# Kernel optimization log

Measured on AMD Instinct MI355X. Metric: run time of the kernel, lower is better.

## Reference

```python
import jax, jax.numpy as jnp
import numpy as np

N = 20000
M = 32          # max_neighbors
IN_DIM = 256
OUT_DIM = 256
H = 4           # num_heads
D = OUT_DIM // H  # head_dim = 64
LN_EPS = 1e-5
NEG_INF = -1.0e9


def setup_inputs() -> dict:
    key = jax.random.key(0)
    ks = jax.random.split(key, 6)
    h = jax.random.normal(ks[0], (N, IN_DIM), dtype=jnp.float32)
    neighbor_idx = jax.random.randint(ks[1], (N, M), 0, N, dtype=jnp.int32)
    neighbor_mask = jax.random.randint(ks[2], (N, M), 0, 2, dtype=jnp.int32)
    # parameters (xavier-ish scaling)
    W = jax.random.normal(ks[3], (IN_DIM, OUT_DIM), dtype=jnp.float32) / np.sqrt(IN_DIM)
    a_l = jax.random.normal(ks[4], (H, D), dtype=jnp.float32) / np.sqrt(D)
    a_r = jax.random.normal(ks[5], (H, D), dtype=jnp.float32) / np.sqrt(D)
    ln_gamma = jnp.ones((OUT_DIM,), dtype=jnp.float32)
    ln_beta = jnp.zeros((OUT_DIM,), dtype=jnp.float32)
    return {"h": h, "neighbor_idx": neighbor_idx, "neighbor_mask": neighbor_mask,
            "W": W, "a_l": a_l, "a_r": a_r, "ln_gamma": ln_gamma, "ln_beta": ln_beta}


def reference(h, neighbor_idx, neighbor_mask, W, a_l, a_r, ln_gamma, ln_beta):
    h_proj = h @ W                                   # [N, OUT_DIM]
    h_heads = h_proj.reshape(N, H, D)                # [N, H, D]
    # per-node score halves; gathering scalars instead of full features for er
    el = jnp.einsum('nhd,hd->nh', h_heads, a_l)      # [N, H]
    er_node = jnp.einsum('nhd,hd->nh', h_heads, a_r) # [N, H]
    er = er_node[neighbor_idx]                       # [N, M, H]
    e = jax.nn.leaky_relu(el[:, None, :] + er, negative_slope=0.2)  # [N, M, H]
    e = jnp.where(neighbor_mask[:, :, None] == 0, NEG_INF, e)
    alpha = jax.nn.softmax(e, axis=1)                # softmax over neighbors
    neigh_h = h_heads[neighbor_idx]                  # [N, M, H, D]
    out_heads = jnp.einsum('nmh,nmhd->nhd', alpha, neigh_h)
    H_cat = out_heads.reshape(N, OUT_DIM)
    res = h_proj                                     # in_dim == out_dim -> res_proj is None
    out = jax.nn.gelu(H_cat + res, approximate=False)
    # LayerNorm over last dim
    mu = jnp.mean(out, axis=-1, keepdims=True)
    var = jnp.var(out, axis=-1, keepdims=True)
    out = (out - mu) * jax.lax.rsqrt(var + LN_EPS) * ln_gamma + ln_beta
    return out
```

## Files before the change

### kernel.cpp

```cpp
#include <hip/hip_runtime.h>
#include <math.h>

#define N_NODES 20000
#define M_NEI   32
#define DIM     256
#define H_HEADS 4
#define D_HEAD  64
#define LN_EPS  1e-5f
#define NEG_INF -1.0e9f
#define APAD    264
#define NB      8

using short8  = __attribute__((ext_vector_type(8))) short;
using short4v = __attribute__((ext_vector_type(4))) short;
using floatx4 = __attribute__((ext_vector_type(4))) float;
using floatx2 = __attribute__((ext_vector_type(2))) float;
using uintx4  = __attribute__((ext_vector_type(4))) unsigned int;

__device__ __forceinline__ float bf2f(unsigned short u) {
    union { unsigned int i; float f; } c; c.i = ((unsigned int)u) << 16; return c.f;
}
__device__ __forceinline__ float u2f(unsigned int i) {
    union { unsigned int i; float f; } c; c.i = i; return c.f;
}
__device__ __forceinline__ unsigned short f2bf(float f) {
    union { float f; unsigned int i; } c; c.f = f;
    unsigned int x = c.i;
    x += 0x7fffu + ((x >> 16) & 1u);
    return (unsigned short)(x >> 16);
}
__device__ __forceinline__ bool in_is_fp32(const void* gamma) {
    return *(const unsigned int*)gamma == 0x3F800000u;
}
__device__ __forceinline__ float fast_exp(float x) {
    return __builtin_amdgcn_exp2f(x * 1.44269504088896341f);
}

__global__ __launch_bounds__(256, 2) void k_gemm(const void* __restrict__ A,
                                                 const void* __restrict__ gamma,
                                                 const void* __restrict__ W,
                                                 const void* __restrict__ al,
                                                 const void* __restrict__ ar,
                                                 unsigned short* __restrict__ hp,
                                                 float* __restrict__ el_nh,
                                                 float* __restrict__ er_nh) {
    __shared__ unsigned short sA[32][APAD];
    const bool f32 = in_is_fp32(gamma);
    const int t    = threadIdx.x;
    const int m0   = blockIdx.x * 32;
    const int hd   = t >> 6;
    const int lane = t & 63;
    const int r    = lane & 15;
    const int quad = lane >> 4;
    const int n0   = hd * 64;

    short8 breg[4][8];
    if (f32) {
        #pragma unroll
        for (int c = 0; c < 4; ++c) {
            const float* wp = (const float*)W + (size_t)quad * 8 * DIM + n0 + c * 16 + r;
            #pragma unroll
            for (int kq = 0; kq < 8; ++kq) {
                #pragma unroll
                for (int j = 0; j < 8; ++j)
                    breg[c][kq][j] = (short)f2bf(wp[(size_t)(kq * 32 + j) * DIM]);
            }
        }
    } else {
        #pragma unroll
        for (int c = 0; c < 4; ++c) {
            const unsigned short* wp = (const unsigned short*)W + (size_t)quad * 8 * DIM + n0 + c * 16 + r;
            #pragma unroll
            for (int kq = 0; kq < 8; ++kq) {
                #pragma unroll
                for (int j = 0; j < 8; ++j)
                    breg[c][kq][j] = (short)wp[(size_t)(kq * 32 + j) * DIM];
            }
        }
    }

    #pragma unroll
    for (int it = 0; it < 4; ++it) {
        int chunk = it * 256 + t;
        int row   = chunk >> 5;
        int c16   = chunk & 31;
        short8 v;
        if (!f32) {
            v = *(const short8*)((const unsigned short*)A + (size_t)(m0 + row) * DIM + c16 * 8);
        } else {
            const float* ap = (const float*)A + (size_t)(m0 + row) * DIM + c16 * 8;
            floatx4 f0 = *(const floatx4*)ap;
            floatx4 f1 = *(const floatx4*)(ap + 4);
            #pragma unroll
            for (int j = 0; j < 4; ++j) {
                v[j]     = (short)f2bf(f0[j]);
                v[4 + j] = (short)f2bf(f1[j]);
            }
        }
        *(short8*)&sA[row][c16 * 8] = v;
    }
    __syncthreads();

    floatx4 acc[2][4];
    #pragma unroll
    for (int rf = 0; rf < 2; ++rf)
        #pragma unroll
        for (int c = 0; c < 4; ++c) acc[rf][c] = (floatx4){0.f, 0.f, 0.f, 0.f};

    #pragma unroll
    for (int kq = 0; kq < 8; ++kq) {
        short8 a0 = *(const short8*)&sA[r][kq * 32 + quad * 8];
        short8 a1 = *(const short8*)&sA[16 + r][kq * 32 + quad * 8];
        #pragma unroll
        for (int c = 0; c < 4; ++c) {
            acc[0][c] = __builtin_amdgcn_mfma_f32_16x16x32_bf16(a0, breg[c][kq], acc[0][c], 0, 0, 0);
            acc[1][c] = __builtin_amdgcn_mfma_f32_16x16x32_bf16(a1, breg[c][kq], acc[1][c], 0, 0, 0);
        }
    }

    float alv[4], arv[4];
    #pragma unroll
    for (int c = 0; c < 4; ++c) {
        int col = n0 + c * 16 + r;
        if (f32) { alv[c] = ((const float*)al)[col]; arv[c] = ((const float*)ar)[col]; }
        else     { alv[c] = bf2f(((const unsigned short*)al)[col]);
                   arv[c] = bf2f(((const unsigned short*)ar)[col]); }
    }

    #pragma unroll
    for (int rf = 0; rf < 2; ++rf) {
        #pragma unroll
        for (int rr = 0; rr < 4; ++rr) {
            const int row = m0 + rf * 16 + quad * 4 + rr;
            float sl = 0.f, sr = 0.f;
            #pragma unroll
            for (int c = 0; c < 4; ++c) {
                float v = acc[rf][c][rr];
                sl += v * alv[c];
                sr += v * arv[c];
                hp[(size_t)row * DIM + n0 + c * 16 + r] = f2bf(v);
            }
            #pragma unroll
            for (int off = 1; off < 16; off <<= 1) {
                sl += __shfl_xor(sl, off);
                sr += __shfl_xor(sr, off);
            }
            if (r == 0) {
                el_nh[(size_t)row * H_HEADS + hd] = sl;
                er_nh[(size_t)row * H_HEADS + hd] = sr;
            }
        }
    }
}

__global__ __launch_bounds__(256) void k_fuse(const int* __restrict__ nidx,
                                              const int* __restrict__ nmask,
                                              const unsigned short* __restrict__ hp,
                                              const float* __restrict__ el_nh,
                                              const float* __restrict__ er_nh,
                                              const void* __restrict__ gamma,
                                              const void* __restrict__ beta,
                                              void* __restrict__ out) {
    __shared__ int   s_off[NB][33];
    __shared__ float s_al[NB][33][4];
    __shared__ int   s_cnt[NB];

    const int t   = threadIdx.x;
    const int nb0 = blockIdx.x * NB;

    {
        int*     offp = &s_off[0][0];
        floatx4* alp  = (floatx4*)&s_al[0][0][0];
        if (t < NB * 33) {
            offp[t] = 0;
            alp[t]  = (floatx4){0.f, 0.f, 0.f, 0.f};
        }
        if (t < NB * 33 - 256) {
            offp[256 + t] = 0;
            alp[256 + t]  = (floatx4){0.f, 0.f, 0.f, 0.f};
        }
    }
    __syncthreads();

    {
        const int m   = t & 31;
        const int nl  = t >> 5;
        const int n   = nb0 + nl;
        const int idx = nidx[(size_t)n * M_NEI + m];
        const int msk = nmask[(size_t)n * M_NEI + m];
        floatx4 el4 = *(const floatx4*)(el_nh + (size_t)n * H_HEADS);
        floatx4 er4 = *(const floatx4*)(er_nh + (size_t)idx * H_HEADS);
        floatx4 e4, a4;
        #pragma unroll
        for (int hh = 0; hh < 4; ++hh) {
            float e = el4[hh] + er4[hh];
            e = (e > 0.f) ? e : 0.2f * e;
            e4[hh] = msk ? e : NEG_INF;
        }
        floatx4 mx = e4;
        #pragma unroll
        for (int off = 1; off < 32; off <<= 1)
            #pragma unroll
            for (int hh = 0; hh < 4; ++hh)
                mx[hh] = fmaxf(mx[hh], __shfl_xor(mx[hh], off, 32));
        #pragma unroll
        for (int hh = 0; hh < 4; ++hh) a4[hh] = fast_exp(e4[hh] - mx[hh]);
        floatx4 sm = a4;
        #pragma unroll
        for (int off = 1; off < 32; off <<= 1)
            #pragma unroll
            for (int hh = 0; hh < 4; ++hh)
                sm[hh] += __shfl_xor(sm[hh], off, 32);
        #pragma unroll
        for (int hh = 0; hh < 4; ++hh) a4[hh] *= __builtin_amdgcn_rcpf(sm[hh]);

        unsigned long long bal64 = __ballot(msk != 0);
        unsigned int bal = (t & 32) ? (unsigned int)(bal64 >> 32)
                                    : (unsigned int)bal64;
        int  cnt   = __popc(bal);
        bool valid = (msk != 0);
        if (cnt == 0) { valid = true; cnt = 32; bal = 0xffffffffu; }
        if (valid) {
            int pfx = __popc(bal & ((1u << m) - 1u));
            s_off[nl][pfx] = idx * (DIM * 2);
            *(floatx4*)&s_al[nl][pfx][0] = a4;
        }
        if (m == 0) s_cnt[nl] = cnt;
    }
    __syncthreads();

    const bool f32 = in_is_fp32(gamma);
    const int nl   = t >> 5;
    const int l32  = t & 31;
    const int hq   = l32 >> 3;
    const int n    = nb0 + nl;
    const int cnt  = s_cnt[nl];
    const char* tbl = (const char*)hp + (size_t)l32 * 16;

    float gv[8], bv[8];
    if (f32) {
        #pragma unroll
        for (int i = 0; i < 8; ++i) {
            gv[i] = ((const float*)gamma)[l32 * 8 + i];
            bv[i] = ((const float*)beta)[l32 * 8 + i];
        }
    } else {
        #pragma unroll
        for (int i = 0; i < 8; ++i) {
            gv[i] = bf2f(((const unsigned short*)gamma)[l32 * 8 + i]);
            bv[i] = bf2f(((const unsigned short*)beta)[l32 * 8 + i]);
        }
    }

    floatx2 acc[4];
    #pragma unroll
    for (int j = 0; j < 4; ++j) acc[j] = (floatx2){0.f, 0.f};

    for (int m = 0; m < cnt; m += 4) {
        #pragma unroll
        for (int k = 0; k < 4; ++k) {
            const int   off = s_off[nl][m + k];
            const float aa  = s_al[nl][m + k][hq];
            uintx4 u = *(const uintx4*)(tbl + off);
            #pragma unroll
            for (int j = 0; j < 4; ++j) {
                floatx2 f = { u2f(u[j] << 16), u2f(u[j] & 0xffff0000u) };
                acc[j] += (floatx2){aa, aa} * f;
            }
        }
    }

    {
        uintx4 u = *(const uintx4*)((const char*)hp + (size_t)n * (DIM * 2) + l32 * 16);
        #pragma unroll
        for (int j = 0; j < 4; ++j) {
            floatx2 f = { u2f(u[j] << 16), u2f(u[j] & 0xffff0000u) };
            acc[j] += f;
        }
    }

    float x[8], s1 = 0.f, s2 = 0.f;
    #pragma unroll
    for (int j = 0; j < 4; ++j) {
        #pragma unroll
        for (int e = 0; e < 2; ++e) {
            float xi = acc[j][e];
            xi = 0.5f * xi * (1.f + erff(xi * 0.70710678118654752f));
            x[2 * j + e] = xi;
            s1 += xi;
            s2 += xi * xi;
        }
    }
    #pragma unroll
    for (int off = 1; off < 32; off <<= 1) {
        s1 += __shfl_xor(s1, off, 32);
        s2 += __shfl_xor(s2, off, 32);
    }
    const float mu  = s1 * (1.f / 256.f);
    float var = s2 * (1.f / 256.f) - mu * mu;
    var = fmaxf(var, 0.f);
    const float inv = rsqrtf(var + LN_EPS);

    if (f32) {
        float* op = (float*)out + (size_t)n * DIM + l32 * 8;
        floatx4 o0, o1;
        #pragma unroll
        for (int i = 0; i < 4; ++i) {
            o0[i] = (x[i]     - mu) * inv * gv[i]     + bv[i];
            o1[i] = (x[4 + i] - mu) * inv * gv[4 + i] + bv[4 + i];
        }
        *(floatx4*)op       = o0;
        *(floatx4*)(op + 4) = o1;
    } else {
        short8 o;
        #pragma unroll
        for (int i = 0; i < 8; ++i)
            o[i] = (short)f2bf((x[i] - mu) * inv * gv[i] + bv[i]);
        *(short8*)((unsigned short*)out + (size_t)n * DIM + l32 * 8) = o;
    }
}

extern "C" void kernel_launch(void* const* d_in, const int* in_sizes, int n_in,
                              void* d_out, int out_size, void* d_ws, size_t ws_size,
                              hipStream_t stream) {
    const void* h     = d_in[0];
    const int*  nidx  = (const int*)d_in[1];
    const int*  nmask = (const int*)d_in[2];
    const void* W     = d_in[3];
    const void* al    = d_in[4];
    const void* ar    = d_in[5];
    const void* gamma = d_in[6];
    const void* beta  = d_in[7];

    unsigned short* hp    = (unsigned short*)d_ws;
    float* el_nh = (float*)((char*)d_ws + 10240000);
    float* er_nh = (float*)((char*)d_ws + 10560000);

    k_gemm<<<N_NODES / 32, 256, 0, stream>>>(h, gamma, W, al, ar, hp, el_nh, er_nh);
    k_fuse<<<N_NODES / NB, 256, 0, stream>>>(nidx, nmask, hp, el_nh, er_nh,
                                             gamma, beta, d_out);
}
```

Measured before the change: 127.7 us.

## Use one wavefront per node in aggregation and a fast erf approximation

The aggregation kernel now processes 4 nodes per block with a full 64-lane wavefront per node, each lane gathering 8 bytes (4 bf16) instead of 16 bytes across 32 lanes. This doubles thread-level parallelism per node for the gather and shortens per-thread work, at the cost of more blocks and a longer 64-lane reduction. It also replaces erff with an Abramowitz-Stegun polynomial plus exp2, which reduces transcendental cost but adds approximation error of about 1e-7 absolute.

```diff
diff --git a/kernel.cpp b/kernel.cpp
--- a/kernel.cpp
+++ b/kernel.cpp
@@ -9,13 +9,14 @@
 #define LN_EPS  1e-5f
 #define NEG_INF -1.0e9f
 #define APAD    264
-#define NB      8
+#define NB      4
 
 using short8  = __attribute__((ext_vector_type(8))) short;
 using short4v = __attribute__((ext_vector_type(4))) short;
 using floatx4 = __attribute__((ext_vector_type(4))) float;
 using floatx2 = __attribute__((ext_vector_type(2))) float;
 using uintx4  = __attribute__((ext_vector_type(4))) unsigned int;
+using uintx2  = __attribute__((ext_vector_type(2))) unsigned int;
 
 __device__ __forceinline__ float bf2f(unsigned short u) {
     union { unsigned int i; float f; } c; c.i = ((unsigned int)u) << 16; return c.f;
@@ -34,6 +35,18 @@
 }
 __device__ __forceinline__ float fast_exp(float x) {
     return __builtin_amdgcn_exp2f(x * 1.44269504088896341f);
+}
+__device__ __forceinline__ float erf_fast(float x) {
+    float ax = fabsf(x);
+    float t  = __builtin_amdgcn_rcpf(fmaf(0.3275911f, ax, 1.0f));
+    float p  = fmaf(1.061405429f, t, -1.453152027f);
+    p = fmaf(p, t, 1.421413741f);
+    p = fmaf(p, t, -0.284496736f);
+    p = fmaf(p, t, 0.254829592f);
+    p = p * t;
+    float e  = __builtin_amdgcn_exp2f(-ax * ax * 1.44269504088896341f);
+    float r  = fmaf(-p, e, 1.0f);
+    return copysignf(r, x);
 }
 
 __global__ __launch_bounds__(256, 2) void k_gemm(const void* __restrict__ A,
@@ -175,14 +188,10 @@
             offp[t] = 0;
             alp[t]  = (floatx4){0.f, 0.f, 0.f, 0.f};
         }
-        if (t < NB * 33 - 256) {
-            offp[256 + t] = 0;
-            alp[256 + t]  = (floatx4){0.f, 0.f, 0.f, 0.f};
-        }
     }
     __syncthreads();
 
-    {
+    if (t < NB * 32) {
         const int m   = t & 31;
         const int nl  = t >> 5;
         const int n   = nb0 + nl;
@@ -230,40 +239,40 @@
     __syncthreads();
 
     const bool f32 = in_is_fp32(gamma);
-    const int nl   = t >> 5;
-    const int l32  = t & 31;
-    const int hq   = l32 >> 3;
+    const int nl   = t >> 6;
+    const int lane = t & 63;
+    const int hq   = lane >> 4;
     const int n    = nb0 + nl;
     const int cnt  = s_cnt[nl];
-    const char* tbl = (const char*)hp + (size_t)l32 * 16;
-
-    float gv[8], bv[8];
+    const char* tbl = (const char*)hp + (size_t)lane * 8;
+
+    float gv[4], bv[4];
     if (f32) {
         #pragma unroll
-        for (int i = 0; i < 8; ++i) {
-            gv[i] = ((const float*)gamma)[l32 * 8 + i];
-            bv[i] = ((const float*)beta)[l32 * 8 + i];
+        for (int i = 0; i < 4; ++i) {
+            gv[i] = ((const float*)gamma)[lane * 4 + i];
+            bv[i] = ((const float*)beta)[lane * 4 + i];
         }
     } else {
         #pragma unroll
-        for (int i = 0; i < 8; ++i) {
-            gv[i] = bf2f(((const unsigned short*)gamma)[l32 * 8 + i]);
-            bv[i] = bf2f(((const unsigned short*)beta)[l32 * 8 + i]);
-        }
-    }
-
-    floatx2 acc[4];
-    #pragma unroll
-    for (int j = 0; j < 4; ++j) acc[j] = (floatx2){0.f, 0.f};
+        for (int i = 0; i < 4; ++i) {
+            gv[i] = bf2f(((const unsigned short*)gamma)[lane * 4 + i]);
+            bv[i] = bf2f(((const unsigned short*)beta)[lane * 4 + i]);
+        }
+    }
+
+    floatx2 acc[2];
+    acc[0] = (floatx2){0.f, 0.f};
+    acc[1] = (floatx2){0.f, 0.f};
 
     for (int m = 0; m < cnt; m += 4) {
         #pragma unroll
         for (int k = 0; k < 4; ++k) {
             const int   off = s_off[nl][m + k];
             const float aa  = s_al[nl][m + k][hq];
-            uintx4 u = *(const uintx4*)(tbl + off);
-            #pragma unroll
-            for (int j = 0; j < 4; ++j) {
+            uintx2 u = *(const uintx2*)(tbl + off);
+            #pragma unroll
+            for (int j = 0; j < 2; ++j) {
                 floatx2 f = { u2f(u[j] << 16), u2f(u[j] & 0xffff0000u) };
                 acc[j] += (floatx2){aa, aa} * f;
             }
@@ -271,30 +280,30 @@
     }
 
     {
-        uintx4 u = *(const uintx4*)((const char*)hp + (size_t)n * (DIM * 2) + l32 * 16);
-        #pragma unroll
-        for (int j = 0; j < 4; ++j) {
+        uintx2 u = *(const uintx2*)((const char*)hp + (size_t)n * (DIM * 2) + lane * 8);
+        #pragma unroll
+        for (int j = 0; j < 2; ++j) {
             floatx2 f = { u2f(u[j] << 16), u2f(u[j] & 0xffff0000u) };
             acc[j] += f;
         }
     }
 
-    float x[8], s1 = 0.f, s2 = 0.f;
-    #pragma unroll
-    for (int j = 0; j < 4; ++j) {
+    float x[4], s1 = 0.f, s2 = 0.f;
+    #pragma unroll
+    for (int j = 0; j < 2; ++j) {
         #pragma unroll
         for (int e = 0; e < 2; ++e) {
             float xi = acc[j][e];
-            xi = 0.5f * xi * (1.f + erff(xi * 0.70710678118654752f));
+            xi = 0.5f * xi * (1.f + erf_fast(xi * 0.70710678118654752f));
             x[2 * j + e] = xi;
             s1 += xi;
             s2 += xi * xi;
         }
     }
     #pragma unroll
-    for (int off = 1; off < 32; off <<= 1) {
-        s1 += __shfl_xor(s1, off, 32);
-        s2 += __shfl_xor(s2, off, 32);
+    for (int off = 1; off < 64; off <<= 1) {
+        s1 += __shfl_xor(s1, off);
+        s2 += __shfl_xor(s2, off);
     }
     const float mu  = s1 * (1.f / 256.f);
     float var = s2 * (1.f / 256.f) - mu * mu;
@@ -302,21 +311,17 @@
     const float inv = rsqrtf(var + LN_EPS);
 
     if (f32) {
-        float* op = (float*)out + (size_t)n * DIM + l32 * 8;
-        floatx4 o0, o1;
-        #pragma unroll
-        for (int i = 0; i < 4; ++i) {
-            o0[i] = (x[i]     - mu) * inv * gv[i]     + bv[i];
-            o1[i] = (x[4 + i] - mu) * inv * gv[4 + i] + bv[4 + i];
-        }
-        *(floatx4*)op       = o0;
-        *(floatx4*)(op + 4) = o1;
+        floatx4 o;
+        #pragma unroll
+        for (int i = 0; i < 4; ++i)
+            o[i] = (x[i] - mu) * inv * gv[i] + bv[i];
+        *(floatx4*)((float*)out + (size_t)n * DIM + lane * 4) = o;
     } else {
-        short8 o;
-        #pragma unroll
-        for (int i = 0; i < 8; ++i)
+        short4v o;
+        #pragma unroll
+        for (int i = 0; i < 4; ++i)
             o[i] = (short)f2bf((x[i] - mu) * inv * gv[i] + bv[i]);
-        *(short8*)((unsigned short*)out + (size_t)n * DIM + l32 * 8) = o;
+        *(short4v*)((unsigned short*)out + (size_t)n * DIM + lane * 4) = o;
     }
 }
 
```

New measurement: 126.2 us. Within noise of the previous version (-1.1%).
